# Kernel tuning notes

Measured on AMD Instinct MI355X. Metric: run time of the kernel, lower is better.

## Reference

```python
import jax, jax.numpy as jnp
import numpy as np
from jax import lax

FX, FY = 518.857, 519.469   # NYU-v2 depth intrinsics (cx/cy unused by forward)
B, H, W = 8, 479, 639       # TRAIN_CROP_SIZE = [W, H]; H+1, W+1 divisible by 4
P = 8                       # even PATCH_SIZE -> box-filter output is [H+1, W+1]
EPS = 1e-6


def _coords():
    # u_u0 = x - W/2, v_v0 = y - H/2, broadcast over [B,1,H,W]
    u = jnp.arange(W, dtype=jnp.float32)[None, None, None, :] - W / 2.0
    v = jnp.arange(H, dtype=jnp.float32)[None, None, :, None] - H / 2.0
    return u, v


def _surface_normal(xyz):
    # xyz: [H, W, 3] -> normals [H, W, 3]
    x, y, z = xyz[..., 0], xyz[..., 1], xyz[..., 2]
    # 9 box-filtered moments in a single depthwise conv (the original does 9 conv2d calls)
    mom = jnp.stack([x * x, x * y, x * z, y * y, y * z, z * z, x, y, z], 0)[None]  # [1,9,H,W]
    kern = jnp.ones((9, 1, P, P), xyz.dtype)
    s = lax.conv_general_dilated(mom, kern, (1, 1), [(P // 2, P // 2)] * 2,
                                 feature_group_count=9)[0]  # [9, H+1, W+1]
    xx, xy, xz, yy, yz, zz, xs, ys, zs = s
    ATA = jnp.stack([xx, xy, xz, xy, yy, yz, xz, yz, zz], -1)  # [H+1, W+1, 9]
    Hp, Wp = ATA.shape[0], ATA.shape[1]
    ATA = ATA.reshape(Hp, Wp, 3, 3) + EPS * jnp.eye(3, dtype=xyz.dtype)
    AT1 = jnp.stack([xs, ys, zs], -1)[..., None]  # [H+1, W+1, 3, 1]
    # original loops over 4x4 sub-patches with overlap=0 -> equivalent full-grid solve
    n = jnp.linalg.solve(ATA, AT1)                # [H+1, W+1, 3, 1]
    n = n / jnp.sqrt(jnp.sum(n * n, axis=2, keepdims=True))
    n = n[:-1, :-1, :, 0]                         # [H, W, 3]
    # orient toward camera: flip where dot(n, xyz) > 0
    flip = jnp.sum(n * xyz, axis=2, keepdims=True) > 0
    return jnp.where(flip, -n, n)


def _fit_normals(depth):
    # depth: [B,1,H,W] -> surface normals [B,3,H,W], zeroed where depth <= 0
    u, v = _coords()
    x = u * depth / FX
    y = v * depth / FY
    xyz = jnp.concatenate([x, y, depth], 1).transpose(0, 2, 3, 1)  # [B,H,W,3]
    sn = jax.vmap(_surface_normal)(xyz).transpose(0, 3, 1, 2)      # [B,3,H,W]
    return jnp.where(depth > 0, sn, 0.0)


def setup_inputs() -> dict:
    key = jax.random.key(0)
    k1, k2 = jax.random.split(key)
    prediction = jax.random.uniform(k1, (B, 1, H, W), jnp.float32)
    gt = jax.random.uniform(k2, (B, 1, H, W), jnp.float32)
    return {"prediction": prediction, "gt": gt}


def reference(prediction, gt):
    return jnp.mean(jnp.abs(_fit_normals(prediction) - _fit_normals(gt)))
```

## Files before the change

### kernel.cpp

```cpp
#include <hip/hip_runtime.h>

#define HH 479
#define WW 639
#define BATCH 8
#define NBLK (20 * 30 * 8)


__device__ __forceinline__ void solve_normal(
    float xx, float xy, float xz, float yy, float yz, float zz,
    float xs, float ys, float zs,
    float a_c, float b_c, float d0,
    float* nx, float* ny, float* nz)
{
    const float EPSV = 1e-6f;
    const float inv64 = 1.0f / 64.0f;
    float hx = xs * inv64, hy = ys * inv64, hz = zs * inv64;
    float cxx = fmaf(-hx, xs, xx) + EPSV;
    float cxy = fmaf(-hx, ys, xy);
    float cxz = fmaf(-hx, zs, xz);
    float cyy = fmaf(-hy, ys, yy) + EPSV;
    float cyz = fmaf(-hy, zs, yz);
    float czz = fmaf(-hz, zs, zz) + EPSV;
    float c00 = fmaf(cyy, czz, -cyz * cyz);
    float c01 = fmaf(cxz, cyz, -cxy * czz);
    float c02 = fmaf(cxy, cyz, -cxz * cyy);
    float c11 = fmaf(cxx, czz, -cxz * cxz);
    float c12 = fmaf(cxy, cxz, -cxx * cyz);
    float c22 = fmaf(cxx, cyy, -cxy * cxy);
    float m0 = fmaf(c00, xs, fmaf(c01, ys, c02 * zs));
    float m1 = fmaf(c01, xs, fmaf(c11, ys, c12 * zs));
    float m2 = fmaf(c02, xs, fmaf(c12, ys, c22 * zs));
    float g  = fmaf(m0, a_c, fmaf(m1, b_c, m2));
    float inv = rsqrtf(fmaf(m0, m0, fmaf(m1, m1, m2 * m2)));
    if (g > 0.0f) inv = -inv;
    if (!(d0 > 0.0f)) inv = 0.0f;
    *nx = m0 * inv; *ny = m1 * inv; *nz = m2 * inv;
}

__global__ __launch_bounds__(256, 6)
void ppal_main(const float* __restrict__ pred, const float* __restrict__ gt,
               double* __restrict__ acc)
{
    const int tx = threadIdx.x;
    const int ty = threadIdx.y;
    const int tid = ty * 16 + tx;
    const int j0 = blockIdx.x * 32;
    const int i0 = blockIdx.y * 16;
    const int b  = blockIdx.z;

    const float invFX = 1.0f / 518.857f;
    const float invFY = 1.0f / 519.469f;

    __shared__ float sd[2][23 * 40];
    __shared__ float cs[624 * 6];
    __shared__ float wsum[4];

    const float* src0 = pred + (size_t)b * (HH * WW);
    const float* src1 = gt   + (size_t)b * (HH * WW);
    for (int idx = tid; idx < 23 * 40; idx += 256) {
        int lr = idx / 40, lc = idx - lr * 40;
        int r = i0 - 4 + lr, c = j0 - 4 + lc;
        bool ok = (lc < 39) && (r >= 0) && (r < HH) && (c >= 0) && (c < WW);
        int off = r * WW + c;
        sd[0][idx] = ok ? src0[off] : 0.0f;
        sd[1][idx] = ok ? src1[off] : 0.0f;
    }

    float aw[9];
#pragma unroll
    for (int m = 0; m < 9; ++m)
        aw[m] = ((float)(j0 + 2 * tx + m - 4) - 319.5f) * invFX;
    const float bc = ((float)(i0 + ty) - 239.5f) * invFY;
    const int ebase = ty * 39 + 2 * tx;

    float n0A[3], n1A[3];
    float contrib = 0.0f;

    __syncthreads();

#pragma unroll
    for (int k = 0; k < 2; ++k) {
        if (tid < 156) {
            int g = tid / 39;
            int c = tid - 39 * g;
            int rb = 8 * (g >> 1) + (g & 1);
            const float* col = &sd[k][c];
            float S1 = 0.f, Sb = 0.f, Sbb = 0.f, T1 = 0.f, Tb = 0.f;
#pragma unroll
            for (int r = 0; r < 8; ++r) {
                int rr = rb + r;
                float d  = col[rr * 40];
                float bv = ((float)(i0 + rr - 4) - 239.5f) * invFY;
                float bd = bv * d;
                T1 += d;  Tb += bd;
                S1  = fmaf(d,  d,  S1);
                Sb  = fmaf(bd, d,  Sb);
                Sbb = fmaf(bd, bd, Sbb);
            }
            {
                float* e = &cs[6 * (rb * 39 + c)];
                *(float2*)(e)     = make_float2(S1, Sb);
                *(float2*)(e + 2) = make_float2(Sbb, T1);
                e[4] = Tb;
            }
#pragma unroll
            for (int s = 1; s < 4; ++s) {
                int i = rb + 2 * s;
                float d0a = col[(i - 2) * 40], d0b = col[(i - 1) * 40];
                float d1a = col[(i + 6) * 40], d1b = col[(i + 7) * 40];
                float b0a = ((float)(i0 + i - 6) - 239.5f) * invFY;
                float b0b = ((float)(i0 + i - 5) - 239.5f) * invFY;
                float b1a = ((float)(i0 + i + 2) - 239.5f) * invFY;
                float b1b = ((float)(i0 + i + 3) - 239.5f) * invFY;
                float bd0a = b0a * d0a, bd0b = b0b * d0b;
                float bd1a = b1a * d1a, bd1b = b1b * d1b;
                T1  += (d1a - d0a) + (d1b - d0b);
                Tb  += (bd1a - bd0a) + (bd1b - bd0b);
                S1  += fmaf(d1a, d1a, -d0a * d0a)
                     + fmaf(d1b, d1b, -d0b * d0b);
                Sb  += fmaf(bd1a, d1a, -bd0a * d0a)
                     + fmaf(bd1b, d1b, -bd0b * d0b);
                Sbb += fmaf(bd1a, bd1a, -bd0a * bd0a)
                     + fmaf(bd1b, bd1b, -bd0b * bd0b);
                float* e = &cs[6 * (i * 39 + c)];
                *(float2*)(e)     = make_float2(S1, Sb);
                *(float2*)(e + 2) = make_float2(Sbb, T1);
                e[4] = Tb;
            }
        }
        __syncthreads();

        {
            float Sxx = 0.f, Sxy = 0.f, Sxz = 0.f, Syy = 0.f, Syz = 0.f;
            float Szz = 0.f, Sxs = 0.f, Sys = 0.f, Szs = 0.f;
#pragma unroll
            for (int m = 1; m < 8; ++m) {
                const float* e = &cs[6 * (ebase + m)];
                float2 p01 = *(const float2*)(e);
                float2 p23 = *(const float2*)(e + 2);
                float  tb  = e[4];
                Szz += p01.x;  Syz += p01.y;  Syy += p23.x;
                Szs += p23.y;  Sys += tb;
                Sxz = fmaf(aw[m],         p01.x, Sxz);
                Sxy = fmaf(aw[m],         p01.y, Sxy);
                Sxs = fmaf(aw[m],         p23.y, Sxs);
                Sxx = fmaf(aw[m] * aw[m], p01.x, Sxx);
            }

            float nn[2][3];
#pragma unroll
            for (int p = 0; p < 2; ++p) {
                int m = (p == 0) ? 0 : 8;
                const float* e = &cs[6 * (ebase + m)];
                float2 p01 = *(const float2*)(e);
                float2 p23 = *(const float2*)(e + 2);
                float  tb  = e[4];
                float xx = fmaf(aw[m] * aw[m], p01.x, Sxx);
                float xy = fmaf(aw[m], p01.y, Sxy);
                float xz = fmaf(aw[m], p01.x, Sxz);
                float yy = Syy + p23.x;
                float yz = Syz + p01.y;
                float zz = Szz + p01.x;
                float xs = fmaf(aw[m], p23.y, Sxs);
                float ys = Sys + tb;
                float zs = Szs + p23.y;
                float d0 = sd[k][(ty + 4) * 40 + (2 * tx + p + 4)];
                solve_normal(xx, xy, xz, yy, yz, zz, xs, ys, zs,
                             aw[4 + p], bc, d0, &nn[p][0], &nn[p][1], &nn[p][2]);
            }
            if (k == 0) {
                n0A[0] = nn[0][0]; n0A[1] = nn[0][1]; n0A[2] = nn[0][2];
                n1A[0] = nn[1][0]; n1A[1] = nn[1][1]; n1A[2] = nn[1][2];
                __syncthreads();
            } else {
                const int i = i0 + ty;
                const bool valid0 = (i < HH);
                const bool valid1 = (i < HH) && (j0 + 2 * tx + 1 < WW);
                float c0 = fabsf(n0A[0] - nn[0][0]) + fabsf(n0A[1] - nn[0][1])
                         + fabsf(n0A[2] - nn[0][2]);
                float c1 = fabsf(n1A[0] - nn[1][0]) + fabsf(n1A[1] - nn[1][1])
                         + fabsf(n1A[2] - nn[1][2]);
                contrib = (valid0 ? c0 : 0.0f) + (valid1 ? c1 : 0.0f);
            }
        }
    }

    float v = contrib;
#pragma unroll
    for (int off = 32; off > 0; off >>= 1) v += __shfl_down(v, off, 64);
    int wid = tid >> 6, lane = tid & 63;
    if (lane == 0) wsum[wid] = v;
    __syncthreads();
    if (tid == 0) {
        double bs = (double)wsum[0] + (double)wsum[1] + (double)wsum[2] + (double)wsum[3];
        int slot = blockIdx.x + 20 * blockIdx.y + 600 * blockIdx.z;
        acc[slot] = bs;
    }
}

__global__ void ppal_finalize(const double* __restrict__ acc, float* __restrict__ out)
{
    int tid = threadIdx.x;
    double v = 0.0;
    for (int s = tid; s < NBLK; s += 256) v += acc[s];
#pragma unroll
    for (int off = 32; off > 0; off >>= 1) v += __shfl_down(v, off, 64);
    __shared__ double wsum[4];
    int wid = tid >> 6, lane = tid & 63;
    if (lane == 0) wsum[wid] = v;
    __syncthreads();
    if (tid == 0)
        out[0] = (float)((wsum[0] + wsum[1] + wsum[2] + wsum[3])
                         * (1.0 / 7345944.0));
}

extern "C" void kernel_launch(void* const* d_in, const int* in_sizes, int n_in,
                              void* d_out, int out_size, void* d_ws, size_t ws_size,
                              hipStream_t stream)
{
    const float* pred = (const float*)d_in[0];
    const float* gt   = (const float*)d_in[1];
    float* out  = (float*)d_out;
    double* acc = (double*)d_ws;

    dim3 grid(20, 30, BATCH);
    dim3 block(16, 16);
    ppal_main<<<grid, block, 0, stream>>>(pred, gt, acc);
    ppal_finalize<<<1, 256, 0, stream>>>(acc, out);
}
```

Before: 106.7 us.

## Split column-sum buffer into per-moment arrays, pad tile stride, simplify row sliding

Replaces the interleaved 6-float column-moment buffer with five separate shared arrays and pads the depth tile row stride from 40 to 41. The goal is to reduce LDS bank conflicts on both the column reads and the strided column-sum stores. The vertical box-sum now splits rows into 4-row groups that slide one row at a time, replacing 2-row groups that slid two rows. It also raises the launch-bounds occupancy hint from 6 to 8 blocks, which may force register spilling.

```diff
diff --git a/kernel.cpp b/kernel.cpp
--- a/kernel.cpp
+++ b/kernel.cpp
@@ -37,7 +37,7 @@
     *nx = m0 * inv; *ny = m1 * inv; *nz = m2 * inv;
 }
 
-__global__ __launch_bounds__(256, 6)
+__global__ __launch_bounds__(256, 8)
 void ppal_main(const float* __restrict__ pred, const float* __restrict__ gt,
                double* __restrict__ acc)
 {
@@ -51,14 +51,14 @@
     const float invFX = 1.0f / 518.857f;
     const float invFY = 1.0f / 519.469f;
 
-    __shared__ float sd[2][23 * 40];
-    __shared__ float cs[624 * 6];
+    __shared__ float sd[2][23 * 41];
+    __shared__ float csS1[624], csSb[624], csSbb[624], csT1[624], csTb[624];
     __shared__ float wsum[4];
 
     const float* src0 = pred + (size_t)b * (HH * WW);
     const float* src1 = gt   + (size_t)b * (HH * WW);
-    for (int idx = tid; idx < 23 * 40; idx += 256) {
-        int lr = idx / 40, lc = idx - lr * 40;
+    for (int idx = tid; idx < 23 * 41; idx += 256) {
+        int lr = idx / 41, lc = idx - lr * 41;
         int r = i0 - 4 + lr, c = j0 - 4 + lc;
         bool ok = (lc < 39) && (r >= 0) && (r < HH) && (c >= 0) && (c < WW);
         int off = r * WW + c;
@@ -83,49 +83,38 @@
         if (tid < 156) {
             int g = tid / 39;
             int c = tid - 39 * g;
-            int rb = 8 * (g >> 1) + (g & 1);
+            int rb = 4 * g;
             const float* col = &sd[k][c];
+            float bv = ((float)(i0 + rb - 4) - 239.5f) * invFY;
             float S1 = 0.f, Sb = 0.f, Sbb = 0.f, T1 = 0.f, Tb = 0.f;
 #pragma unroll
             for (int r = 0; r < 8; ++r) {
-                int rr = rb + r;
-                float d  = col[rr * 40];
-                float bv = ((float)(i0 + rr - 4) - 239.5f) * invFY;
-                float bd = bv * d;
+                float d  = col[(rb + r) * 41];
+                float bvr = fmaf((float)r, invFY, bv);
+                float bd = bvr * d;
                 T1 += d;  Tb += bd;
                 S1  = fmaf(d,  d,  S1);
                 Sb  = fmaf(bd, d,  Sb);
                 Sbb = fmaf(bd, bd, Sbb);
             }
-            {
-                float* e = &cs[6 * (rb * 39 + c)];
-                *(float2*)(e)     = make_float2(S1, Sb);
-                *(float2*)(e + 2) = make_float2(Sbb, T1);
-                e[4] = Tb;
-            }
+            int e = rb * 39 + c;
+            csS1[e] = S1; csSb[e] = Sb; csSbb[e] = Sbb;
+            csT1[e] = T1; csTb[e] = Tb;
 #pragma unroll
             for (int s = 1; s < 4; ++s) {
-                int i = rb + 2 * s;
-                float d0a = col[(i - 2) * 40], d0b = col[(i - 1) * 40];
-                float d1a = col[(i + 6) * 40], d1b = col[(i + 7) * 40];
-                float b0a = ((float)(i0 + i - 6) - 239.5f) * invFY;
-                float b0b = ((float)(i0 + i - 5) - 239.5f) * invFY;
-                float b1a = ((float)(i0 + i + 2) - 239.5f) * invFY;
-                float b1b = ((float)(i0 + i + 3) - 239.5f) * invFY;
-                float bd0a = b0a * d0a, bd0b = b0b * d0b;
-                float bd1a = b1a * d1a, bd1b = b1b * d1b;
-                T1  += (d1a - d0a) + (d1b - d0b);
-                Tb  += (bd1a - bd0a) + (bd1b - bd0b);
-                S1  += fmaf(d1a, d1a, -d0a * d0a)
-                     + fmaf(d1b, d1b, -d0b * d0b);
-                Sb  += fmaf(bd1a, d1a, -bd0a * d0a)
-                     + fmaf(bd1b, d1b, -bd0b * d0b);
-                Sbb += fmaf(bd1a, bd1a, -bd0a * bd0a)
-                     + fmaf(bd1b, bd1b, -bd0b * bd0b);
-                float* e = &cs[6 * (i * 39 + c)];
-                *(float2*)(e)     = make_float2(S1, Sb);
-                *(float2*)(e + 2) = make_float2(Sbb, T1);
-                e[4] = Tb;
+                float d0 = col[(rb + s - 1) * 41];
+                float d1 = col[(rb + s + 7) * 41];
+                float b0 = fmaf((float)(s - 1), invFY, bv);
+                float b1 = fmaf((float)(s + 7), invFY, bv);
+                float bd0 = b0 * d0, bd1 = b1 * d1;
+                T1 += d1 - d0;
+                Tb += bd1 - bd0;
+                S1  += fmaf(d1,  d1,  -d0  * d0);
+                Sb  += fmaf(bd1, d1,  -bd0 * d0);
+                Sbb += fmaf(bd1, bd1, -bd0 * bd0);
+                e += 39;
+                csS1[e] = S1; csSb[e] = Sb; csSbb[e] = Sbb;
+                csT1[e] = T1; csTb[e] = Tb;
             }
         }
         __syncthreads();
@@ -135,36 +124,40 @@
             float Szz = 0.f, Sxs = 0.f, Sys = 0.f, Szs = 0.f;
 #pragma unroll
             for (int m = 1; m < 8; ++m) {
-                const float* e = &cs[6 * (ebase + m)];
-                float2 p01 = *(const float2*)(e);
-                float2 p23 = *(const float2*)(e + 2);
-                float  tb  = e[4];
-                Szz += p01.x;  Syz += p01.y;  Syy += p23.x;
-                Szs += p23.y;  Sys += tb;
-                Sxz = fmaf(aw[m],         p01.x, Sxz);
-                Sxy = fmaf(aw[m],         p01.y, Sxy);
-                Sxs = fmaf(aw[m],         p23.y, Sxs);
-                Sxx = fmaf(aw[m] * aw[m], p01.x, Sxx);
+                int e = ebase + m;
+                float s1  = csS1[e];
+                float sb  = csSb[e];
+                float sbb = csSbb[e];
+                float t1  = csT1[e];
+                float tb  = csTb[e];
+                Szz += s1;  Syz += sb;  Syy += sbb;
+                Szs += t1;  Sys += tb;
+                Sxz = fmaf(aw[m],         s1, Sxz);
+                Sxy = fmaf(aw[m],         sb, Sxy);
+                Sxs = fmaf(aw[m],         t1, Sxs);
+                Sxx = fmaf(aw[m] * aw[m], s1, Sxx);
             }
 
             float nn[2][3];
 #pragma unroll
             for (int p = 0; p < 2; ++p) {
                 int m = (p == 0) ? 0 : 8;
-                const float* e = &cs[6 * (ebase + m)];
-                float2 p01 = *(const float2*)(e);
-                float2 p23 = *(const float2*)(e + 2);
-                float  tb  = e[4];
-                float xx = fmaf(aw[m] * aw[m], p01.x, Sxx);
-                float xy = fmaf(aw[m], p01.y, Sxy);
-                float xz = fmaf(aw[m], p01.x, Sxz);
-                float yy = Syy + p23.x;
-                float yz = Syz + p01.y;
-                float zz = Szz + p01.x;
-                float xs = fmaf(aw[m], p23.y, Sxs);
+                int e = ebase + m;
+                float s1  = csS1[e];
+                float sb  = csSb[e];
+                float sbb = csSbb[e];
+                float t1  = csT1[e];
+                float tb  = csTb[e];
+                float xx = fmaf(aw[m] * aw[m], s1, Sxx);
+                float xy = fmaf(aw[m], sb, Sxy);
+                float xz = fmaf(aw[m], s1, Sxz);
+                float yy = Syy + sbb;
+                float yz = Syz + sb;
+                float zz = Szz + s1;
+                float xs = fmaf(aw[m], t1, Sxs);
                 float ys = Sys + tb;
-                float zs = Szs + p23.y;
-                float d0 = sd[k][(ty + 4) * 40 + (2 * tx + p + 4)];
+                float zs = Szs + t1;
+                float d0 = sd[k][(ty + 4) * 41 + (2 * tx + p + 4)];
                 solve_normal(xx, xy, xz, yy, yz, zz, xs, ys, zs,
                              aw[4 + p], bc, d0, &nn[p][0], &nn[p][1], &nn[p][2]);
             }
```

Result: faster. 99.11 us (-7.1%).
